# Kernel optimization log

Hardware: AMD Instinct MI355X
Metric: run time of the kernel (lower is better)

Reference implementation:

```python
import jax, jax.numpy as jnp
import numpy as np

N = 50000      # nodes
E = 800000     # edges (before self-loops)
H = 4          # heads
C = 64         # hidden channels per head
CLS = 10       # len(bins)+1
D_IN = 64      # input feature dim
NEG_SLOPE = 0.2


def setup_inputs() -> dict:
    key = jax.random.key(0)
    ks = jax.random.split(key, 24)
    inp = {
        "x": jax.random.normal(ks[0], (N, D_IN), jnp.float32),
        "edge_index": jax.random.randint(ks[1], (2, E), 0, N),
    }
    dims = [(D_IN, C), (H * C, C), (H * C, C), (H * C, C), (H * C, CLS)]
    k = 2
    for l, (din, dout) in enumerate(dims):
        sc = 1.0 / np.sqrt(din)
        inp[f"W{l}"] = jax.random.normal(ks[k], (din, H * dout), jnp.float32) * sc; k += 1
        inp[f"as{l}"] = jax.random.normal(ks[k], (H, dout), jnp.float32) * sc; k += 1
        inp[f"ad{l}"] = jax.random.normal(ks[k], (H, dout), jnp.float32) * sc; k += 1
        inp[f"b{l}"] = jnp.zeros((H * dout,), jnp.float32)
    return inp


def gat_layer(x, src, dst, W, a_s, a_d, b):
    # PyG GATConv (concat=True): h = x W -> [N,H,Ch]
    Hh, Ch = a_s.shape
    h = (x @ W).reshape(-1, Hh, Ch)
    asn = (h * a_s).sum(-1)                      # [N,H]
    adn = (h * a_d).sum(-1)                      # [N,H]
    e = jax.nn.leaky_relu(asn[src] + adn[dst], NEG_SLOPE)   # [Et,H]
    m = jax.ops.segment_max(e, dst, num_segments=N)         # softmax over in-edges per dst
    ex = jnp.exp(e - m[dst])
    s = jax.ops.segment_sum(ex, dst, num_segments=N)
    alpha = ex / (s[dst] + 1e-16)                # [Et,H]
    out = jax.ops.segment_sum(alpha[:, :, None] * h[src], dst, num_segments=N)
    return out.reshape(-1, Hh * Ch) + b


def reference(x, edge_index, W0, as0, ad0, b0, W1, as1, ad1, b1,
              W2, as2, ad2, b2, W3, as3, ad3, b3, W4, as4, ad4, b4):
    loop = jnp.arange(N, dtype=edge_index.dtype)  # GATConv add_self_loops=True
    src = jnp.concatenate([edge_index[0], loop])
    dst = jnp.concatenate([edge_index[1], loop])
    params = [(W0, as0, ad0, b0), (W1, as1, ad1, b1), (W2, as2, ad2, b2),
              (W3, as3, ad3, b3), (W4, as4, ad4, b4)]
    for W, a_s, a_d, b in params:
        x = jax.nn.relu(gat_layer(x, src, dst, W, a_s, a_d, b))
        # dropout(p=0.5) is identity in eval mode (training=False)
    return x
```

## Files before the change

kernel.cpp:

```cpp
#include <hip/hip_runtime.h>
#include <hip/hip_bf16.h>
#include <math.h>

#define N_NODES 50000
#define N_PAD   50048
#define N_EDGES 800000
#define HEADS 4

typedef __attribute__((ext_vector_type(8))) _Float16 half8_t;
typedef __attribute__((ext_vector_type(4))) _Float16 half4_t;
typedef __attribute__((ext_vector_type(4))) float f32x4;

__device__ inline void split2(float v, _Float16& p0, _Float16& p1) {
    p0 = (_Float16)v;
    p1 = (_Float16)(v - (float)p0);
}



__global__ void init_deg_kernel(int* __restrict__ deg) {
    int i = blockIdx.x * blockDim.x + threadIdx.x;
    if (i < N_NODES) deg[i] = 1;
}

__global__ void hist_kernel(const int* __restrict__ dst, int* __restrict__ deg) {
    int i = blockIdx.x * blockDim.x + threadIdx.x;
    if (i < N_EDGES) atomicAdd(&deg[dst[i]], 1);
}

__global__ __launch_bounds__(1024) void scan_kernel(const int* __restrict__ deg,
                                                    int* __restrict__ rowptr,
                                                    int* __restrict__ cursor) {
    __shared__ int wsums[16];
    const int t = threadIdx.x;
    const int wv = t >> 6, ln = t & 63;
    const int WCHUNK = (N_NODES + 15) / 16;
    const int base = wv * WCHUNK;
    int lim = base + WCHUNK; if (lim > N_NODES) lim = N_NODES;

    int tot = 0;
    for (int i = base + ln; i < lim; i += 64) tot += deg[i];
#pragma unroll
    for (int o = 1; o < 64; o <<= 1) tot += __shfl_xor(tot, o);
    if (ln == 0) wsums[wv] = tot;
    __syncthreads();

    int run = 0;
    for (int w = 0; w < wv; ++w) run += wsums[w];

    for (int i0 = base; i0 < lim; i0 += 64) {
        int i = i0 + ln;
        int d = (i < lim) ? deg[i] : 0;
        int sc = d;
#pragma unroll
        for (int o = 1; o < 64; o <<= 1) {
            int v = __shfl_up(sc, o);
            if (ln >= o) sc += v;
        }
        if (i < lim) {
            int val = run + sc - d;
            rowptr[i] = val;
            cursor[i] = val;
        }
        run += __shfl(sc, 63);
    }
    if (t == 1023) rowptr[N_NODES] = run;
}

__global__ void scatter_kernel(const int* __restrict__ src, const int* __restrict__ dst,
                               int* __restrict__ cursor, int* __restrict__ col) {
    int i = blockIdx.x * blockDim.x + threadIdx.x;
    if (i < N_EDGES) {
        int d = dst[i];
        int pos = atomicAdd(&cursor[d], 1);
        col[pos] = src[i];
    } else if (i < N_EDGES + N_NODES) {
        int n = i - N_EDGES;
        int pos = atomicAdd(&cursor[n], 1);
        col[pos] = n;
    }
}


__global__ void x_split_kernel(const float* __restrict__ x, _Float16* __restrict__ pl,
                               size_t pstride) {
    int i = blockIdx.x * blockDim.x + threadIdx.x;
    if (i >= N_NODES * 64) return;
    int n = i >> 6, k = i & 63;
    _Float16 a, b;
    split2(x[i], a, b);
    size_t off = (size_t)(k >> 5) * ((size_t)N_PAD * 32) + (size_t)n * 32 +
                 ((((k >> 3) & 3) ^ (n & 3)) << 3) + (k & 7);
    pl[off] = a;
    pl[pstride + off] = b;
}

__global__ void w_split_kernel(const float* __restrict__ W, _Float16* __restrict__ wt,
                               int K, int NC) {
    int t = blockIdx.x * blockDim.x + threadIdx.x;
    int c = t >> 8, k = t & 255;
    float v = (k < K && c < NC) ? W[k * NC + c] : 0.f;
    _Float16 a, b;
    split2(v, a, b);
    size_t off = (size_t)(k >> 5) * 8192 + (size_t)c * 32 +
                 ((((k >> 3) & 3) ^ (c & 3)) << 3) + (k & 7);
    wt[off] = a;
    wt[65536 + off] = b;
}


template <int FUSE_ATTN>
__global__ __launch_bounds__(256) void gemm_mfma_kernel(
        const _Float16* __restrict__ Apl, size_t apstride,
        const _Float16* __restrict__ Wt,
        _Float16* __restrict__ hpl, size_t hstride,
        float* __restrict__ C, int K, int NC,
        const float* __restrict__ as_flat, const float* __restrict__ ad_flat,
        float* __restrict__ asn, float* __restrict__ adn) {
    __shared__ __align__(16) _Float16 lds[2][16384];

    const int tid = threadIdx.x;
    const int lane = tid & 63;
    const int wave = tid >> 6;
    const int wr = (wave >> 1) * 64;
    const int wc = (wave & 1) * 64;
    const int m0 = blockIdx.x * 128;
    const int n0 = blockIdx.y * 128;

    f32x4 acc[4][4];
#pragma unroll
    for (int i = 0; i < 4; ++i)
#pragma unroll
        for (int j = 0; j < 4; ++j) acc[i][j] = (f32x4){0.f, 0.f, 0.f, 0.f};

    const _Float16* gptr[8];
    size_t ktstep;
    {
        const _Float16* sbase;
        int rowbase;
        if (wave < 2) {
            sbase = Apl + (size_t)wave * apstride;
            rowbase = m0;
            ktstep = (size_t)N_PAD * 32;
        } else {
            sbase = Wt + (size_t)(wave - 2) * 65536;
            rowbase = n0;
            ktstep = 8192;
        }
#pragma unroll
        for (int it = 0; it < 8; ++it) {
            int idx = it * 64 + lane;
            gptr[it] = sbase + (size_t)(rowbase + (idx >> 2)) * 32 + (idx & 3) * 8;
        }
    }

    const int cswz = ((lane >> 4) ^ (lane & 3)) << 3;
    const int KT = K >> 5;

#pragma unroll
    for (int it = 0; it < 8; ++it) {
        __builtin_amdgcn_global_load_lds(
            (const __attribute__((address_space(1))) void*)gptr[it],
            (__attribute__((address_space(3))) void*)((char*)&lds[0][0] + wave * 8192 + it * 1024),
            16, 0, 0);
    }

    for (int kt = 0; kt < KT; ++kt) {
        __syncthreads();

        if (kt + 1 < KT) {
            char* dstw = (char*)&lds[(kt + 1) & 1][0] + wave * 8192;
#pragma unroll
            for (int it = 0; it < 8; ++it) {
                __builtin_amdgcn_global_load_lds(
                    (const __attribute__((address_space(1))) void*)(gptr[it] + (size_t)(kt + 1) * ktstep),
                    (__attribute__((address_space(3))) void*)(dstw + it * 1024),
                    16, 0, 0);
            }
        }

        const _Float16* Ab = &lds[kt & 1][0];
        const _Float16* Bb = Ab + 8192;

        half8_t bf[2][4];
#pragma unroll
        for (int p = 0; p < 2; ++p)
#pragma unroll
            for (int j = 0; j < 4; ++j) {
                int r = wc + j * 16 + (lane & 15);
                bf[p][j] = *(const half8_t*)(Bb + p * 4096 + r * 32 + cswz);
            }
#pragma unroll
        for (int i = 0; i < 4; ++i) {
            int r = wr + i * 16 + (lane & 15);
            half8_t af0 = *(const half8_t*)(Ab + r * 32 + cswz);
            half8_t af1 = *(const half8_t*)(Ab + 4096 + r * 32 + cswz);
#pragma unroll
            for (int j = 0; j < 4; ++j) {
                f32x4 c = acc[i][j];
                c = __builtin_amdgcn_mfma_f32_16x16x32_f16(af0, bf[1][j], c, 0, 0, 0);
                c = __builtin_amdgcn_mfma_f32_16x16x32_f16(af1, bf[0][j], c, 0, 0, 0);
                c = __builtin_amdgcn_mfma_f32_16x16x32_f16(af0, bf[0][j], c, 0, 0, 0);
                acc[i][j] = c;
            }
        }
    }

    const int rbase = m0 + wr + (lane >> 4) * 4;
    const int cbase = n0 + wc + (lane & 15);

    if (FUSE_ATTN) {
#pragma unroll
        for (int i = 0; i < 4; ++i)
#pragma unroll
            for (int j = 0; j < 4; ++j) {
                int gcol = cbase + j * 16;
#pragma unroll
                for (int r4 = 0; r4 < 4; ++r4) {
                    int grow = rbase + i * 16 + r4;
                    if (grow < N_NODES) {
                        _Float16 a, b;
                        split2(acc[i][j][r4], a, b);
                        size_t off = (size_t)grow * 256 + gcol;
                        hpl[off] = a;
                        hpl[hstride + off] = b;
                    }
                }
            }
        const int hd_out = (n0 + wc) >> 6;
        float as_v[4], ad_v[4];
#pragma unroll
        for (int j = 0; j < 4; ++j) {
            int gc = cbase + j * 16;
            as_v[j] = as_flat[gc];
            ad_v[j] = ad_flat[gc];
        }
#pragma unroll
        for (int i = 0; i < 4; ++i)
#pragma unroll
            for (int r4 = 0; r4 < 4; ++r4) {
                float ps = 0.f, pd = 0.f;
#pragma unroll
                for (int j = 0; j < 4; ++j) {
                    float v = acc[i][j][r4];
                    ps += v * as_v[j];
                    pd += v * ad_v[j];
                }
#pragma unroll
                for (int o = 1; o < 16; o <<= 1) {
                    ps += __shfl_xor(ps, o);
                    pd += __shfl_xor(pd, o);
                }
                if ((lane & 15) == 0) {
                    int grow = rbase + i * 16 + r4;
                    if (grow < N_NODES) {
                        asn[grow * 4 + hd_out] = ps;
                        adn[grow * 4 + hd_out] = pd;
                    }
                }
            }
    } else {
#pragma unroll
        for (int i = 0; i < 4; ++i)
#pragma unroll
            for (int j = 0; j < 4; ++j) {
                int gcol = cbase + j * 16;
                if (gcol >= NC) continue;
#pragma unroll
                for (int r4 = 0; r4 < 4; ++r4) {
                    int grow = rbase + i * 16 + r4;
                    if (grow < N_NODES) C[(size_t)grow * NC + gcol] = acc[i][j][r4];
                }
            }
    }
}


__global__ void attn_coef_kernel(const float* __restrict__ h,
                                 const float* __restrict__ a_s,
                                 const float* __restrict__ a_d,
                                 float* __restrict__ asn, float* __restrict__ adn,
                                 int CH) {
    int t = blockIdx.x * blockDim.x + threadIdx.x;
    if (t >= N_NODES * HEADS) return;
    int n = t >> 2;
    int hd = t & 3;
    const float* hp = h + (size_t)n * HEADS * CH + hd * CH;
    const float* sp = a_s + hd * CH;
    const float* dp = a_d + hd * CH;
    float s1 = 0.f, s2 = 0.f;
    for (int c = 0; c < CH; c += 2) {
        float2 hv = *reinterpret_cast<const float2*>(&hp[c]);
        float2 av = *reinterpret_cast<const float2*>(&sp[c]);
        float2 dv = *reinterpret_cast<const float2*>(&dp[c]);
        s1 += hv.x * av.x + hv.y * av.y;
        s2 += hv.x * dv.x + hv.y * dv.y;
    }
    asn[t] = s1;
    adn[t] = s2;
}


__global__ __launch_bounds__(256) void aggregate64_kernel(
        const _Float16* __restrict__ hpl, size_t hstride,
        const float* __restrict__ asn, const float* __restrict__ adn,
        const int* __restrict__ rowptr, const int* __restrict__ col,
        const float* __restrict__ bias,
        _Float16* __restrict__ pl, size_t pstride) {
    const int n = (blockIdx.x << 2) + (threadIdx.x >> 6);
    const int lane = threadIdx.x & 63;
    const int hd = lane >> 4;
    const int e16 = lane & 15;
    const int pbase = lane & 48;

    const int start = rowptr[n];
    const int end = rowptr[n + 1];
    const float adv = adn[(n << 2) | hd];

    float m = -INFINITY, s = 0.f;
    float a0 = 0.f, a1 = 0.f, a2 = 0.f, a3 = 0.f;

    for (int e0 = start; e0 < end; e0 += 16) {
        int e = e0 + e16;
        int srcl = n;
        float ev = -INFINITY;
        if (e < end) {
            srcl = col[e];
            float t = asn[(srcl << 2) | hd] + adv;
            ev = (t > 0.f) ? t : 0.2f * t;
        }
        float bm = ev;
#pragma unroll
        for (int o = 1; o < 16; o <<= 1) bm = fmaxf(bm, __shfl_xor(bm, o));
        float mn = fmaxf(m, bm);
        float scale = __expf(m - mn);
        float p = __expf(ev - mn);
        float ps = p;
#pragma unroll
        for (int o = 1; o < 16; o <<= 1) ps += __shfl_xor(ps, o);
        s = s * scale + ps;
        a0 *= scale; a1 *= scale; a2 *= scale; a3 *= scale;
        m = mn;

        int cnt = end - e0; if (cnt > 16) cnt = 16;
        int cnt4 = (cnt + 3) & ~3;
        for (int j0 = 0; j0 < cnt4; j0 += 4) {
            int sj[4]; float pj[4];
#pragma unroll
            for (int j = 0; j < 4; ++j) {
                sj[j] = __shfl(srcl, j0 + j);
                pj[j] = __shfl(p, pbase + j0 + j);
            }
            half4_t h0[4], h1[4];
#pragma unroll
            for (int j = 0; j < 4; ++j) {
                const _Float16* hp = hpl + (size_t)sj[j] * 256 + (lane << 2);
                h0[j] = *(const half4_t*)hp;
                h1[j] = *(const half4_t*)(hp + hstride);
            }
#pragma unroll
            for (int j = 0; j < 4; ++j) {
                a0 += pj[j] * ((float)h0[j][0] + (float)h1[j][0]);
                a1 += pj[j] * ((float)h0[j][1] + (float)h1[j][1]);
                a2 += pj[j] * ((float)h0[j][2] + (float)h1[j][2]);
                a3 += pj[j] * ((float)h0[j][3] + (float)h1[j][3]);
            }
        }
    }

    float sd = s + 1e-16f;
    const float* bp = bias + (lane << 2);
    float v0 = fmaxf(a0 / sd + bp[0], 0.f);
    float v1 = fmaxf(a1 / sd + bp[1], 0.f);
    float v2 = fmaxf(a2 / sd + bp[2], 0.f);
    float v3 = fmaxf(a3 / sd + bp[3], 0.f);

    _Float16 s0a, s0b, s1a, s1b, s2a, s2b, s3a, s3b;
    split2(v0, s0a, s0b);
    split2(v1, s1a, s1b);
    split2(v2, s2a, s2b);
    split2(v3, s3a, s3b);
    half4_t o0, o1;
    o0[0] = s0a; o0[1] = s1a; o0[2] = s2a; o0[3] = s3a;
    o1[0] = s0b; o1[1] = s1b; o1[2] = s2b; o1[3] = s3b;

    const int kt = lane >> 3;
    const int cp = ((lane >> 1) & 3) ^ (n & 3);
    const int inner = (lane & 1) << 2;
    size_t off = (size_t)kt * ((size_t)N_PAD * 32) + (size_t)n * 32 + (cp << 3) + inner;
    *(half4_t*)(pl + off) = o0;
    *(half4_t*)(pl + pstride + off) = o1;
}


template <int CH>
__global__ __launch_bounds__(256) void aggregate_out_kernel(
        const float* __restrict__ h, const float* __restrict__ asn,
        const float* __restrict__ adn, const int* __restrict__ rowptr,
        const int* __restrict__ col, const float* __restrict__ bias,
        float* __restrict__ out) {
    constexpr int HC = HEADS * CH;
    __shared__ float2 pair_lds[HEADS][32];

    const int n = blockIdx.x;
    const int hd = threadIdx.x >> 6;
    const int lane = threadIdx.x & 63;
    const int el = lane & 31;
    const int hdoff = hd * CH + lane;

    const int start = rowptr[n];
    const int end = rowptr[n + 1];
    const float adv = adn[(n << 2) | hd];

    float m = -INFINITY, s = 0.f;
    float accv[4] = {0.f, 0.f, 0.f, 0.f};

    for (int e0 = start; e0 < end; e0 += 32) {
        int e = e0 + el;
        bool valid = (lane < 32) && (e < end);
        int srcl = n;
        float ev = -INFINITY;
        if (valid) {
            srcl = col[e];
            float t = asn[(srcl << 2) | hd] + adv;
            ev = (t > 0.f) ? t : 0.2f * t;
        }
        float bm = ev;
#pragma unroll
        for (int o = 1; o < 64; o <<= 1) bm = fmaxf(bm, __shfl_xor(bm, o));
        float mn = fmaxf(m, bm);
        float scale = __expf(m - mn);
        float p = __expf(ev - mn);
        float ps = p;
#pragma unroll
        for (int o = 1; o < 64; o <<= 1) ps += __shfl_xor(ps, o);
        s = s * scale + ps;
#pragma unroll
        for (int c = 0; c < 4; ++c) accv[c] *= scale;
        m = mn;

        if (lane < 32) pair_lds[hd][lane] = make_float2(__int_as_float(srcl), p);

        int cnt = end - e0; if (cnt > 32) cnt = 32;
        int cnt8 = (cnt + 7) & ~7;
        for (int i0 = 0; i0 < cnt8; i0 += 8) {
            int sv[8]; float pv[8];
#pragma unroll
            for (int j = 0; j < 8; ++j) {
                float2 pr = pair_lds[hd][i0 + j];
                sv[j] = __float_as_int(pr.x);
                pv[j] = pr.y;
            }
            float hv[8];
#pragma unroll
            for (int j = 0; j < 8; ++j)
                hv[j] = (lane < CH) ? h[(size_t)sv[j] * HC + hdoff] : 0.f;
#pragma unroll
            for (int j = 0; j < 8; ++j) accv[j & 3] += pv[j] * hv[j];
        }
    }

    if (lane < CH) {
        float acc = (accv[0] + accv[1]) + (accv[2] + accv[3]);
        float v = acc / (s + 1e-16f) + bias[hd * CH + lane];
        out[n * HC + hd * CH + lane] = fmaxf(v, 0.f);
    }
}


extern "C" void kernel_launch(void* const* d_in, const int* in_sizes, int n_in,
                              void* d_out, int out_size, void* d_ws, size_t ws_size,
                              hipStream_t stream) {
    const float* x_in = (const float*)d_in[0];
    const int* ei = (const int*)d_in[1];
    const int* src = ei;
    const int* dst = ei + N_EDGES;

    const float *W[5], *AS[5], *AD[5], *BI[5];
    for (int l = 0; l < 5; ++l) {
        W[l]  = (const float*)d_in[2 + l * 4 + 0];
        AS[l] = (const float*)d_in[2 + l * 4 + 1];
        AD[l] = (const float*)d_in[2 + l * 4 + 2];
        BI[l] = (const float*)d_in[2 + l * 4 + 3];
    }

    const size_t PSTRIDE = (size_t)N_PAD * 256;
    _Float16* planes = (_Float16*)d_ws;
    _Float16* hpl = planes + 2 * PSTRIDE;
    float* Hb   = (float*)(hpl + 2 * PSTRIDE);
    float* asn  = Hb + (size_t)N_NODES * 40;
    float* adn  = asn + (size_t)N_NODES * HEADS;
    int* rowptr = (int*)(adn + (size_t)N_NODES * HEADS);
    int* cursor = rowptr + (N_NODES + 1);
    int* col    = cursor + N_NODES;
    _Float16* wt = (_Float16*)(((uintptr_t)(col + N_EDGES + N_NODES) + 15) & ~(uintptr_t)15);

    init_deg_kernel<<<(N_NODES + 255) / 256, 256, 0, stream>>>(cursor);
    hist_kernel<<<(N_EDGES + 255) / 256, 256, 0, stream>>>(dst, cursor);
    scan_kernel<<<1, 1024, 0, stream>>>(cursor, rowptr, cursor);
    scatter_kernel<<<(N_EDGES + N_NODES + 255) / 256, 256, 0, stream>>>(src, dst, cursor, col);

    for (int l = 0; l < 5; ++l) {
        int Kl = (l == 0) ? 64 : 256;
        int NCl = (l == 4) ? 40 : 256;
        w_split_kernel<<<256, 256, 0, stream>>>(W[l], wt + (size_t)l * 2 * 65536, Kl, NCl);
    }
    x_split_kernel<<<(N_NODES * 64 + 255) / 256, 256, 0, stream>>>(x_in, planes, PSTRIDE);

    for (int l = 0; l < 5; ++l) {
        const int K = (l == 0) ? 64 : 256;
        const int NC = (l == 4) ? 40 : 256;
        dim3 ggrid(N_PAD / 128, (NC + 127) / 128);
        const _Float16* wl = wt + (size_t)l * 2 * 65536;
        if (l < 4) {
            gemm_mfma_kernel<1><<<ggrid, 256, 0, stream>>>(
                planes, PSTRIDE, wl, hpl, PSTRIDE, nullptr, K, NC,
                AS[l], AD[l], asn, adn);
            aggregate64_kernel<<<N_NODES / 4, 256, 0, stream>>>(
                hpl, PSTRIDE, asn, adn, rowptr, col, BI[l], planes, PSTRIDE);
        } else {
            gemm_mfma_kernel<0><<<ggrid, 256, 0, stream>>>(
                planes, PSTRIDE, wl, nullptr, 0, Hb, K, NC,
                AS[l], AD[l], asn, adn);
            attn_coef_kernel<<<(N_NODES * HEADS + 255) / 256, 256, 0, stream>>>(
                Hb, AS[l], AD[l], asn, adn, 10);
            aggregate_out_kernel<10><<<N_NODES, 256, 0, stream>>>(
                Hb, asn, adn, rowptr, col, BI[l], (float*)d_out);
        }
    }
    (void)in_sizes; (void)n_in; (void)out_size; (void)ws_size;
}
```

Before: 913.9 us.

## Store GEMM output as fp32 and pack four nodes per block in final aggregation

The fused GEMM now writes hidden features as a single fp32 buffer instead of two fp16 split planes, and the 64-channel aggregation gathers one float4 per edge rather than two half4 loads it then recombines. The last-layer aggregation is rewritten to handle four nodes per block with one wave per node, 16-edge chunks and shuffle-based softmax instead of LDS pairs, which removes block-level idling. Gather bytes per edge are unchanged, but fewer load instructions and conversions are issued, and the fp16 split write pass is dropped.

```diff
diff --git a/kernel.cpp b/kernel.cpp
--- a/kernel.cpp
+++ b/kernel.cpp
@@ -113,7 +113,6 @@
 __global__ __launch_bounds__(256) void gemm_mfma_kernel(
         const _Float16* __restrict__ Apl, size_t apstride,
         const _Float16* __restrict__ Wt,
-        _Float16* __restrict__ hpl, size_t hstride,
         float* __restrict__ C, int K, int NC,
         const float* __restrict__ as_flat, const float* __restrict__ ad_flat,
         float* __restrict__ asn, float* __restrict__ adn) {
@@ -218,13 +217,7 @@
 #pragma unroll
                 for (int r4 = 0; r4 < 4; ++r4) {
                     int grow = rbase + i * 16 + r4;
-                    if (grow < N_NODES) {
-                        _Float16 a, b;
-                        split2(acc[i][j][r4], a, b);
-                        size_t off = (size_t)grow * 256 + gcol;
-                        hpl[off] = a;
-                        hpl[hstride + off] = b;
-                    }
+                    if (grow < N_NODES) C[(size_t)grow * 256 + gcol] = acc[i][j][r4];
                 }
             }
         const int hd_out = (n0 + wc) >> 6;
@@ -302,7 +295,7 @@
 
 
 __global__ __launch_bounds__(256) void aggregate64_kernel(
-        const _Float16* __restrict__ hpl, size_t hstride,
+        const float* __restrict__ h,
         const float* __restrict__ asn, const float* __restrict__ adn,
         const int* __restrict__ rowptr, const int* __restrict__ col,
         const float* __restrict__ bias,
@@ -351,19 +344,16 @@
                 sj[j] = __shfl(srcl, j0 + j);
                 pj[j] = __shfl(p, pbase + j0 + j);
             }
-            half4_t h0[4], h1[4];
-#pragma unroll
-            for (int j = 0; j < 4; ++j) {
-                const _Float16* hp = hpl + (size_t)sj[j] * 256 + (lane << 2);
-                h0[j] = *(const half4_t*)hp;
-                h1[j] = *(const half4_t*)(hp + hstride);
-            }
-#pragma unroll
-            for (int j = 0; j < 4; ++j) {
-                a0 += pj[j] * ((float)h0[j][0] + (float)h1[j][0]);
-                a1 += pj[j] * ((float)h0[j][1] + (float)h1[j][1]);
-                a2 += pj[j] * ((float)h0[j][2] + (float)h1[j][2]);
-                a3 += pj[j] * ((float)h0[j][3] + (float)h1[j][3]);
+            float4 hv[4];
+#pragma unroll
+            for (int j = 0; j < 4; ++j)
+                hv[j] = *reinterpret_cast<const float4*>(h + (size_t)sj[j] * 256 + (lane << 2));
+#pragma unroll
+            for (int j = 0; j < 4; ++j) {
+                a0 += pj[j] * hv[j].x;
+                a1 += pj[j] * hv[j].y;
+                a2 += pj[j] * hv[j].z;
+                a3 += pj[j] * hv[j].w;
             }
         }
     }
@@ -393,77 +383,73 @@
 }
 
 
-template <int CH>
-__global__ __launch_bounds__(256) void aggregate_out_kernel(
-        const float* __restrict__ h, const float* __restrict__ asn,
-        const float* __restrict__ adn, const int* __restrict__ rowptr,
-        const int* __restrict__ col, const float* __restrict__ bias,
-        float* __restrict__ out) {
-    constexpr int HC = HEADS * CH;
-    __shared__ float2 pair_lds[HEADS][32];
-
-    const int n = blockIdx.x;
-    const int hd = threadIdx.x >> 6;
+__global__ __launch_bounds__(256) void aggregate_out10_kernel(
+        const float* __restrict__ h,
+        const float* __restrict__ asn, const float* __restrict__ adn,
+        const int* __restrict__ rowptr, const int* __restrict__ col,
+        const float* __restrict__ bias, float* __restrict__ out) {
+    const int n = (blockIdx.x << 2) + (threadIdx.x >> 6);
     const int lane = threadIdx.x & 63;
-    const int el = lane & 31;
-    const int hdoff = hd * CH + lane;
+    const int hd16 = lane >> 4;
+    const int e16 = lane & 15;
+    const bool cvalid = lane < 40;
+    const int hc = ((cvalid ? lane : 0) * 205) >> 11;
 
     const int start = rowptr[n];
     const int end = rowptr[n + 1];
-    const float adv = adn[(n << 2) | hd];
-
-    float m = -INFINITY, s = 0.f;
-    float accv[4] = {0.f, 0.f, 0.f, 0.f};
-
-    for (int e0 = start; e0 < end; e0 += 32) {
-        int e = e0 + el;
-        bool valid = (lane < 32) && (e < end);
+    const float adv = adn[(n << 2) | hd16];
+
+    float m = -INFINITY, s = 0.f, a0 = 0.f, a1 = 0.f;
+
+    for (int e0 = start; e0 < end; e0 += 16) {
+        int e = e0 + e16;
         int srcl = n;
         float ev = -INFINITY;
-        if (valid) {
+        if (e < end) {
             srcl = col[e];
-            float t = asn[(srcl << 2) | hd] + adv;
+            float t = asn[(srcl << 2) | hd16] + adv;
             ev = (t > 0.f) ? t : 0.2f * t;
         }
         float bm = ev;
 #pragma unroll
-        for (int o = 1; o < 64; o <<= 1) bm = fmaxf(bm, __shfl_xor(bm, o));
+        for (int o = 1; o < 16; o <<= 1) bm = fmaxf(bm, __shfl_xor(bm, o));
         float mn = fmaxf(m, bm);
         float scale = __expf(m - mn);
         float p = __expf(ev - mn);
         float ps = p;
 #pragma unroll
-        for (int o = 1; o < 64; o <<= 1) ps += __shfl_xor(ps, o);
+        for (int o = 1; o < 16; o <<= 1) ps += __shfl_xor(ps, o);
         s = s * scale + ps;
-#pragma unroll
-        for (int c = 0; c < 4; ++c) accv[c] *= scale;
         m = mn;
 
-        if (lane < 32) pair_lds[hd][lane] = make_float2(__int_as_float(srcl), p);
-
-        int cnt = end - e0; if (cnt > 32) cnt = 32;
-        int cnt8 = (cnt + 7) & ~7;
-        for (int i0 = 0; i0 < cnt8; i0 += 8) {
-            int sv[8]; float pv[8];
-#pragma unroll
-            for (int j = 0; j < 8; ++j) {
-                float2 pr = pair_lds[hd][i0 + j];
-                sv[j] = __float_as_int(pr.x);
-                pv[j] = pr.y;
-            }
-            float hv[8];
-#pragma unroll
-            for (int j = 0; j < 8; ++j)
-                hv[j] = (lane < CH) ? h[(size_t)sv[j] * HC + hdoff] : 0.f;
-#pragma unroll
-            for (int j = 0; j < 8; ++j) accv[j & 3] += pv[j] * hv[j];
-        }
-    }
-
-    if (lane < CH) {
-        float acc = (accv[0] + accv[1]) + (accv[2] + accv[3]);
-        float v = acc / (s + 1e-16f) + bias[hd * CH + lane];
-        out[n * HC + hd * CH + lane] = fmaxf(v, 0.f);
+        float sc_c = __shfl(scale, hc * 16);
+        a0 *= sc_c;
+        a1 *= sc_c;
+
+        int cnt = end - e0; if (cnt > 16) cnt = 16;
+        int cnt4 = (cnt + 3) & ~3;
+        for (int j0 = 0; j0 < cnt4; j0 += 4) {
+            int sj[4]; float pj[4];
+#pragma unroll
+            for (int j = 0; j < 4; ++j) {
+                sj[j] = __shfl(srcl, j0 + j);
+                pj[j] = __shfl(p, hc * 16 + j0 + j);
+            }
+            float hv[4];
+#pragma unroll
+            for (int j = 0; j < 4; ++j)
+                hv[j] = cvalid ? h[(size_t)sj[j] * 40 + lane] : 0.f;
+            a0 += pj[0] * hv[0];
+            a1 += pj[1] * hv[1];
+            a0 += pj[2] * hv[2];
+            a1 += pj[3] * hv[3];
+        }
+    }
+
+    float sd = __shfl(s, hc * 16) + 1e-16f;
+    if (cvalid) {
+        float v = (a0 + a1) / sd + bias[lane];
+        out[(size_t)n * 40 + lane] = fmaxf(v, 0.f);
     }
 }
 
@@ -486,9 +472,8 @@
 
     const size_t PSTRIDE = (size_t)N_PAD * 256;
     _Float16* planes = (_Float16*)d_ws;
-    _Float16* hpl = planes + 2 * PSTRIDE;
-    float* Hb   = (float*)(hpl + 2 * PSTRIDE);
-    float* asn  = Hb + (size_t)N_NODES * 40;
+    float* hbuf = (float*)(planes + 2 * PSTRIDE);
+    float* asn  = hbuf + (size_t)N_NODES * 256;
     float* adn  = asn + (size_t)N_NODES * HEADS;
     int* rowptr = (int*)(adn + (size_t)N_NODES * HEADS);
     int* cursor = rowptr + (N_NODES + 1);
@@ -503,7 +488,7 @@
     for (int l = 0; l < 5; ++l) {
         int Kl = (l == 0) ? 64 : 256;
         int NCl = (l == 4) ? 40 : 256;
-        w_split_kernel<<<256, 256, 0, stream>>>(W[l], wt + (size_t)l * 2 * 65536, Kl, NCl);
+        w_split_kernel<<<256, 256, 0, stream>>>(W[l], wt + (size_t)l * 131072, Kl, NCl);
     }
     x_split_kernel<<<(N_NODES * 64 + 255) / 256, 256, 0, stream>>>(x_in, planes, PSTRIDE);
 
@@ -511,21 +496,19 @@
         const int K = (l == 0) ? 64 : 256;
         const int NC = (l == 4) ? 40 : 256;
         dim3 ggrid(N_PAD / 128, (NC + 127) / 128);
-        const _Float16* wl = wt + (size_t)l * 2 * 65536;
+        const _Float16* wl = wt + (size_t)l * 131072;
         if (l < 4) {
             gemm_mfma_kernel<1><<<ggrid, 256, 0, stream>>>(
-                planes, PSTRIDE, wl, hpl, PSTRIDE, nullptr, K, NC,
-                AS[l], AD[l], asn, adn);
+                planes, PSTRIDE, wl, hbuf, K, NC, AS[l], AD[l], asn, adn);
             aggregate64_kernel<<<N_NODES / 4, 256, 0, stream>>>(
-                hpl, PSTRIDE, asn, adn, rowptr, col, BI[l], planes, PSTRIDE);
+                hbuf, asn, adn, rowptr, col, BI[l], planes, PSTRIDE);
         } else {
             gemm_mfma_kernel<0><<<ggrid, 256, 0, stream>>>(
-                planes, PSTRIDE, wl, nullptr, 0, Hb, K, NC,
-                AS[l], AD[l], asn, adn);
+                planes, PSTRIDE, wl, hbuf, K, NC, AS[l], AD[l], asn, adn);
             attn_coef_kernel<<<(N_NODES * HEADS + 255) / 256, 256, 0, stream>>>(
-                Hb, AS[l], AD[l], asn, adn, 10);
-            aggregate_out_kernel<10><<<N_NODES, 256, 0, stream>>>(
-                Hb, asn, adn, rowptr, col, BI[l], (float*)d_out);
+                hbuf, AS[l], AD[l], asn, adn, 10);
+            aggregate_out10_kernel<<<N_NODES / 4, 256, 0, stream>>>(
+                hbuf, asn, adn, rowptr, col, BI[l], (float*)d_out);
         }
     }
     (void)in_sizes; (void)n_in; (void)out_size; (void)ws_size;
```

Measured after the change: 842.6 us. 7.8% less time.
